# Performance work log

Hardware: AMD Instinct MI355X
Metric: run time of the kernel (lower is better)

Reference implementation:

```python
import jax, jax.numpy as jnp
import numpy as np
from jax import lax

H, W = 480, 640
EPS = 1e-20
DN = ('NCHW', 'OIHW', 'NCHW')


def _nconv(x, c, w_raw, b, pad):
    # Normalized convolution: positive weights via softplus (EnforcePos hook).
    w = jax.nn.softplus(w_raw)                     # (O, I, kh, kw)
    pads = [(pad, pad), (pad, pad)]
    denom = lax.conv_general_dilated(c, w, (1, 1), pads, dimension_numbers=DN)
    nomin = lax.conv_general_dilated(x * c, w, (1, 1), pads, dimension_numbers=DN)
    out = nomin / (denom + EPS) + b.reshape(1, -1, 1, 1)
    s = w.reshape(w.shape[0], -1).sum(-1).reshape(1, -1, 1, 1)  # per-out-ch weight sum
    return out, denom / s


def _pool2(x, c):
    # max_pool2d(c, 2, 2, return_indices=True) + gather of x at the argmax
    # locations (vectorized form of the per-(b,c) Python gather loops).
    B, C, h, w = c.shape
    cb = c.reshape(B, C, h // 2, 2, w // 2, 2).transpose(0, 1, 2, 4, 3, 5).reshape(B, C, h // 2, w // 2, 4)
    xb = x.reshape(B, C, h // 2, 2, w // 2, 2).transpose(0, 1, 2, 4, 3, 5).reshape(B, C, h // 2, w // 2, 4)
    idx = jnp.argmax(cb, axis=-1)
    c_ds = jnp.max(cb, axis=-1)
    x_ds = jnp.take_along_axis(xb, idx[..., None], axis=-1)[..., 0]
    return x_ds, c_ds


def _up2(a):
    return jnp.repeat(jnp.repeat(a, 2, axis=2), 2, axis=3)


def _adaptive_mat(n_in, n_out):
    # 1D adaptive average pooling as a (n_out, n_in) averaging matrix
    i = np.arange(n_out)
    st = (i * n_in) // n_out
    en = -((-(i + 1) * n_in) // n_out)  # ceil division
    M = np.zeros((n_out, n_in), np.float32)
    for r in range(n_out):
        M[r, st[r]:en[r]] = 1.0 / (en[r] - st[r])
    return jnp.asarray(M)


def _forward(S, w1, b1, w2, b2, w3, b3, w4, b4, w5, b5, w6, b6, w65, b65, w7, b7):
    c0 = (S > 0.01).astype(S.dtype)
    x1, c1 = _nconv(S, c0, w1, b1, 2)
    x1, c1 = _nconv(x1, c1, w2, b2, 2)
    x1, c1 = _nconv(x1, c1, w3, b3, 2)
    # scale 1/2
    x1_ds, c1_ds = _pool2(x1, c1)
    c1_ds = c1_ds / 4
    x2_ds, c2_ds = _nconv(x1_ds, c1_ds, w2, b2, 2)
    x2_ds, c2_ds = _nconv(x2_ds, c2_ds, w3, b3, 2)
    # scale 1/4
    x2_dss, c2_dss = _pool2(x2_ds, c2_ds)
    c2_dss = c2_dss / 4
    x3_ds, c3_ds = _nconv(x2_dss, c2_dss, w2, b2, 2)
    # scale 1/8
    x3_dss, c3_dss = _pool2(x3_ds, c3_ds)
    c3_dss = c3_dss / 4
    x4_ds, c4_ds = _nconv(x3_dss, c3_dss, w2, b2, 2)
    # decoder
    x4, c4 = _up2(x4_ds), _up2(c4_ds)
    x34_ds, c34_ds = _nconv(jnp.concatenate((x3_ds, x4), 1), jnp.concatenate((c3_ds, c4), 1), w4, b4, 1)
    x34, c34 = _up2(x34_ds), _up2(c34_ds)
    x23_ds, c23_ds = _nconv(jnp.concatenate((x2_ds, x34), 1), jnp.concatenate((c2_ds, c34), 1), w5, b5, 1)
    x23, c23 = _up2(x23_ds), _up2(c23_ds)
    xo, co = _nconv(jnp.concatenate((x23, x1), 1), jnp.concatenate((c23, c1), 1), w6, b6, 0)  # shrinks by 2
    xo, co = _nconv(xo, co, w65, b65, 1)
    xo, co = _nconv(xo, co, w7, b7, 0)
    Mh = _adaptive_mat(xo.shape[2], H)
    Mw = _adaptive_mat(xo.shape[3], W)
    return jnp.einsum('oi,bcij,pj->bcop', Mh, xo, Mw)


def setup_inputs() -> dict:
    key = jax.random.key(0)
    ks = jax.random.split(key, 20)
    B = 8
    d = {
        'fout': jax.random.normal(ks[0], (B, 3, H, W), jnp.float32),
        'S': jax.random.uniform(ks[1], (B, 1, H, W), jnp.float32),
        'K': jax.random.normal(ks[2], (B, 3, 3), jnp.float32),
    }
    shapes = {'w1': (4, 1, 5, 5), 'w2': (4, 4, 5, 5), 'w3': (4, 4, 5, 5),
              'w4': (4, 8, 3, 3), 'w5': (4, 8, 3, 3), 'w6': (4, 8, 3, 3),
              'w65': (4, 4, 3, 3), 'w7': (1, 4, 1, 1)}
    i = 3
    for name, sh in shapes.items():
        d[name] = 0.1 * jax.random.normal(ks[i], sh, jnp.float32)
        i += 1
        d['b' + name[1:]] = 0.01 * jax.random.normal(ks[i], (sh[0],), jnp.float32)
        i += 1
    return d


def reference(fout, S, K, w1, b1, w2, b2, w3, b3, w4, b4, w5, b5, w6, b6, w65, b65, w7, b7):
    # fout and K are accepted but unused by the original forward.
    return _forward(S, w1, b1, w2, b2, w3, b3, w4, b4, w5, b5, w6, b6, w65, b65, w7, b7)
```

## Files before the change

kernel.cpp:

```cpp
#include <hip/hip_runtime.h>


#define EPSN 1e-20f

typedef float v2f __attribute__((ext_vector_type(2)));

__device__ __forceinline__ float softplusf(float x) {
    return fmaxf(x, 0.f) + log1pf(expf(-fabsf(x)));
}
__device__ __forceinline__ float rcpf(float x) { return __builtin_amdgcn_rcpf(x); }

__device__ __forceinline__ void wsum4(const float4* s_w4, int n, int tid, float4* dst)
{
    if (tid < 64) {
        float4 a = make_float4(0.f, 0.f, 0.f, 0.f);
        for (int i = tid; i < n; i += 64) {
            float4 w = s_w4[i];
            a.x += w.x; a.y += w.y; a.z += w.z; a.w += w.w;
        }
        #pragma unroll
        for (int off = 32; off; off >>= 1) {
            a.x += __shfl_xor(a.x, off);
            a.y += __shfl_xor(a.y, off);
            a.z += __shfl_xor(a.z, off);
            a.w += __shfl_xor(a.w, off);
        }
        if (tid == 0) *dst = a;
    }
}

__device__ __forceinline__ void tap4(v2f v, v2f w01, v2f w23, v2f* a)
{
    asm("v_pk_fma_f32 %0, %1, %2, %0 op_sel:[0,0,0] op_sel_hi:[1,0,1]"
        : "+v"(a[0]) : "v"(w01), "v"(v));
    asm("v_pk_fma_f32 %0, %1, %2, %0 op_sel:[0,0,0] op_sel_hi:[1,0,1]"
        : "+v"(a[1]) : "v"(w23), "v"(v));
    asm("v_pk_fma_f32 %0, %1, %2, %0 op_sel:[0,1,0] op_sel_hi:[1,1,1]"
        : "+v"(a[2]) : "v"(w01), "v"(v));
    asm("v_pk_fma_f32 %0, %1, %2, %0 op_sel:[0,1,0] op_sel_hi:[1,1,1]"
        : "+v"(a[3]) : "v"(w23), "v"(v));
}
#define TAP2(W01, W23, VA, VB)  tap4((VA),(W01),(W23),aA); tap4((VB),(W01),(W23),aB);

#define NC_EPI(A, XO, CO)                                            \
    XO.x = A[2].x*rcpf(A[0].x+EPSN)+bias.x; CO.x = A[0].x*rs0;       \
    XO.y = A[2].y*rcpf(A[0].y+EPSN)+bias.y; CO.y = A[0].y*rs1;       \
    XO.z = A[3].x*rcpf(A[1].x+EPSN)+bias.z; CO.z = A[1].x*rs2;       \
    XO.w = A[3].y*rcpf(A[1].y+EPSN)+bias.w; CO.w = A[1].y*rs3;

#define NC_STORE_PACKED(HOUT, WOUT)                                         \
    {                                                                       \
        const int oh = oh0 + ty, ow = ow0 + 2 * tx;                         \
        if (oh < (HOUT) && ow < (WOUT)) {                                   \
            float4 bias = s_bias, ssum = s_sum;                             \
            float rs0=rcpf(ssum.x), rs1=rcpf(ssum.y),                       \
                  rs2=rcpf(ssum.z), rs3=rcpf(ssum.w);                       \
            size_t t = ((size_t)b * (HOUT) + oh) * (WOUT) + ow;             \
            float4 xo, co;                                                  \
            NC_EPI(aA, xo, co)                                              \
            xout4[t] = xo; cout4[t] = co;                                   \
            if (ow + 1 < (WOUT)) {                                          \
                NC_EPI(aB, xo, co)                                          \
                xout4[t+1] = xo; cout4[t+1] = co;                           \
            }                                                               \
        }                                                                   \
    }

__global__ __launch_bounds__(256) void nconv5_first(
    const float* __restrict__ S,
    const float* __restrict__ wraw, const float* __restrict__ braw,
    float4* __restrict__ xout4, float4* __restrict__ cout4,
    int Hh, int Ww)
{
    __shared__ v2f sdE[20][19], sdO[20][19];
    __shared__ float4 s_w4[25];
    __shared__ float4 s_sum, s_bias;
    const int b = blockIdx.z;
    const int oh0 = blockIdx.y * 16, ow0 = blockIdx.x * 32;
    const int tx = threadIdx.x, ty = threadIdx.y, tid = ty * 16 + tx;

    if (tid < 25) {
        float4 w;
        w.x = softplusf(wraw[tid]);      w.y = softplusf(wraw[25 + tid]);
        w.z = softplusf(wraw[50 + tid]); w.w = softplusf(wraw[75 + tid]);
        s_w4[tid] = w;
    }
    if (tid == 0) s_bias = make_float4(braw[0], braw[1], braw[2], braw[3]);
    __syncthreads();

    for (int i = tid; i < 20 * 18; i += 256) {
        int ly = i / 18, j = i - ly * 18;
        int ih = oh0 - 2 + ly, iw = ow0 - 2 + 2 * j;
        float s0 = 0.f, s1 = 0.f;
        if ((unsigned)ih < (unsigned)Hh && iw >= 0 && iw < Ww - 1) {
            float2 t = *(const float2*)&S[((size_t)b * Hh + ih) * Ww + iw];
            s0 = t.x; s1 = t.y;
        }
        float c0 = (s0 > 0.01f) ? 1.f : 0.f;
        float c1 = (s1 > 0.01f) ? 1.f : 0.f;
        sdE[ly][j] = (v2f){c0, s0 * c0};
        sdO[ly][j] = (v2f){c1, s1 * c1};
    }
    wsum4(s_w4, 25, tid, &s_sum);
    __syncthreads();

    v2f aA[4] = {}, aB[4] = {};
    #pragma unroll
    for (int kj = 0; kj < 5; ++kj) {
        const v2f* rE = &sdE[ty + kj][tx];
        const v2f* rO = &sdO[ty + kj][tx];
        v2f e0 = rE[0], o0 = rO[0], e1 = rE[1], o1 = rO[1], e2 = rE[2], o2 = rO[2];
        const v2f* wr = (const v2f*)&s_w4[kj * 5];
        TAP2(wr[0], wr[1], e0, o0)
        TAP2(wr[2], wr[3], o0, e1)
        TAP2(wr[4], wr[5], e1, o1)
        TAP2(wr[6], wr[7], o1, e2)
        TAP2(wr[8], wr[9], e2, o2)
    }
    NC_STORE_PACKED(Hh, Ww)
}

template<bool POOL>
__global__ __launch_bounds__(256) void nconv5p4(
    const float4* __restrict__ xin4, const float4* __restrict__ cin4,
    const float* __restrict__ wraw, const float* __restrict__ braw,
    float4* __restrict__ xout4, float4* __restrict__ cout4,
    float4* __restrict__ xo_p, float4* __restrict__ co_p,
    int Hh, int Ww)
{
    __shared__ v2f sdE[4][20][19], sdO[4][20][19];
    __shared__ float4 s_w4[100];
    __shared__ float4 s_sum, s_bias;
    const int b = blockIdx.z;
    const int oh0 = blockIdx.y * 16, ow0 = blockIdx.x * 32;
    const int tx = threadIdx.x, ty = threadIdx.y, tid = ty * 16 + tx;

    if (tid < 100) {
        float4 w;
        w.x = softplusf(wraw[tid]);       w.y = softplusf(wraw[100 + tid]);
        w.z = softplusf(wraw[200 + tid]); w.w = softplusf(wraw[300 + tid]);
        s_w4[tid] = w;
    }
    if (tid == 0) s_bias = make_float4(braw[0], braw[1], braw[2], braw[3]);
    __syncthreads();

    const float4 z = make_float4(0.f, 0.f, 0.f, 0.f);
    for (int i = tid; i < 20 * 18; i += 256) {
        int ly = i / 18, j = i - ly * 18;
        int ih = oh0 - 2 + ly, iw = ow0 - 2 + 2 * j;
        float4 cA = z, xA = z, cB = z, xB = z;
        if ((unsigned)ih < (unsigned)Hh) {
            size_t rb = ((size_t)b * Hh + ih) * Ww;
            if ((unsigned)iw < (unsigned)Ww)       { cA = cin4[rb + iw];     xA = xin4[rb + iw]; }
            if ((unsigned)(iw + 1) < (unsigned)Ww) { cB = cin4[rb + iw + 1]; xB = xin4[rb + iw + 1]; }
        }
        sdE[0][ly][j] = (v2f){cA.x, xA.x * cA.x};
        sdE[1][ly][j] = (v2f){cA.y, xA.y * cA.y};
        sdE[2][ly][j] = (v2f){cA.z, xA.z * cA.z};
        sdE[3][ly][j] = (v2f){cA.w, xA.w * cA.w};
        sdO[0][ly][j] = (v2f){cB.x, xB.x * cB.x};
        sdO[1][ly][j] = (v2f){cB.y, xB.y * cB.y};
        sdO[2][ly][j] = (v2f){cB.z, xB.z * cB.z};
        sdO[3][ly][j] = (v2f){cB.w, xB.w * cB.w};
    }
    wsum4(s_w4, 100, tid, &s_sum);
    __syncthreads();

    v2f aA[4] = {}, aB[4] = {};
    #pragma unroll 1
    for (int ci = 0; ci < 4; ++ci) {
        #pragma unroll
        for (int kj = 0; kj < 5; ++kj) {
            const v2f* rE = &sdE[ci][ty + kj][tx];
            const v2f* rO = &sdO[ci][ty + kj][tx];
            v2f e0 = rE[0], o0 = rO[0], e1 = rE[1], o1 = rO[1], e2 = rE[2], o2 = rO[2];
            const v2f* wr = (const v2f*)&s_w4[ci * 25 + kj * 5];
            TAP2(wr[0], wr[1], e0, o0)
            TAP2(wr[2], wr[3], o0, e1)
            TAP2(wr[4], wr[5], e1, o1)
            TAP2(wr[6], wr[7], o1, e2)
            TAP2(wr[8], wr[9], e2, o2)
        }
    }

    const int oh = oh0 + ty, ow = ow0 + 2 * tx;
    float4 bias = s_bias, ssum = s_sum;
    float rs0 = rcpf(ssum.x), rs1 = rcpf(ssum.y),
          rs2 = rcpf(ssum.z), rs3 = rcpf(ssum.w);
    float4 xoA, coA, xoB, coB;
    NC_EPI(aA, xoA, coA)
    NC_EPI(aB, xoB, coB)
    const bool rowok = oh < Hh, colA = ow < Ww, colB = ow + 1 < Ww;
    if (rowok && colA) {
        size_t t = ((size_t)b * Hh + oh) * Ww + ow;
        xout4[t] = xoA; cout4[t] = coA;
        if (colB) { xout4[t + 1] = xoB; cout4[t + 1] = coB; }
    }
    if (POOL) {
        float4 cb = coA, xb = xoA;
        if (coB.x > cb.x) { cb.x = coB.x; xb.x = xoB.x; }
        if (coB.y > cb.y) { cb.y = coB.y; xb.y = xoB.y; }
        if (coB.z > cb.z) { cb.z = coB.z; xb.z = xoB.z; }
        if (coB.w > cb.w) { cb.w = coB.w; xb.w = xoB.w; }
        float4 cb2, xb2;
        cb2.x = __shfl_down(cb.x, 16); xb2.x = __shfl_down(xb.x, 16);
        cb2.y = __shfl_down(cb.y, 16); xb2.y = __shfl_down(xb.y, 16);
        cb2.z = __shfl_down(cb.z, 16); xb2.z = __shfl_down(xb.z, 16);
        cb2.w = __shfl_down(cb.w, 16); xb2.w = __shfl_down(xb.w, 16);
        if (!(ty & 1) && rowok && colA) {
            if (cb2.x > cb.x) { cb.x = cb2.x; xb.x = xb2.x; }
            if (cb2.y > cb.y) { cb.y = cb2.y; xb.y = xb2.y; }
            if (cb2.z > cb.z) { cb.z = cb2.z; xb.z = xb2.z; }
            if (cb2.w > cb.w) { cb.w = cb2.w; xb.w = xb2.w; }
            cb.x *= 0.25f; cb.y *= 0.25f; cb.z *= 0.25f; cb.w *= 0.25f;
            size_t tp = ((size_t)b * (Hh >> 1) + (oh >> 1)) * (Ww >> 1) + (ow >> 1);
            xo_p[tp] = xb; co_p[tp] = cb;
        }
    }
}

template<bool UP_FIRST, int PAD>
__global__ __launch_bounds__(256) void nconv3cat(
    const float4* __restrict__ xd4, const float4* __restrict__ cd4,
    const float4* __restrict__ xu4, const float4* __restrict__ cu4,
    const float* __restrict__ wraw, const float* __restrict__ braw,
    float4* __restrict__ xout4, float4* __restrict__ cout4,
    int Hin, int Win)
{
    __shared__ v2f sdE[4][18][18], sdO[4][18][18];
    __shared__ v2f sup[4][10][19];
    __shared__ float4 s_w4[72];
    __shared__ float4 s_sum, s_bias;

    const int Hout = Hin - 2 + 2 * PAD, Wout = Win - 2 + 2 * PAD;
    const int Hu = Hin / 2, Wu = Win / 2;
    const int b = blockIdx.z;
    const int oh0 = blockIdx.y * 16, ow0 = blockIdx.x * 32;
    const int tx = threadIdx.x, ty = threadIdx.y, tid = ty * 16 + tx;

    if (tid < 72) {
        float4 w;
        w.x = softplusf(wraw[tid]);       w.y = softplusf(wraw[72 + tid]);
        w.z = softplusf(wraw[144 + tid]); w.w = softplusf(wraw[216 + tid]);
        s_w4[tid] = w;
    }
    if (tid == 0) s_bias = make_float4(braw[0], braw[1], braw[2], braw[3]);
    __syncthreads();

    const float4 z = make_float4(0.f, 0.f, 0.f, 0.f);
    for (int i = tid; i < 18 * 17; i += 256) {
        int ly = i / 17, j = i - ly * 17;
        int ih = oh0 - PAD + ly, iw = ow0 - PAD + 2 * j;
        float4 cA = z, xA = z, cB = z, xB = z;
        if ((unsigned)ih < (unsigned)Hin) {
            size_t rb = ((size_t)b * Hin + ih) * Win;
            if ((unsigned)iw < (unsigned)Win)       { cA = cd4[rb + iw];     xA = xd4[rb + iw]; }
            if ((unsigned)(iw + 1) < (unsigned)Win) { cB = cd4[rb + iw + 1]; xB = xd4[rb + iw + 1]; }
        }
        sdE[0][ly][j] = (v2f){cA.x, xA.x * cA.x};
        sdE[1][ly][j] = (v2f){cA.y, xA.y * cA.y};
        sdE[2][ly][j] = (v2f){cA.z, xA.z * cA.z};
        sdE[3][ly][j] = (v2f){cA.w, xA.w * cA.w};
        sdO[0][ly][j] = (v2f){cB.x, xB.x * cB.x};
        sdO[1][ly][j] = (v2f){cB.y, xB.y * cB.y};
        sdO[2][ly][j] = (v2f){cB.z, xB.z * cB.z};
        sdO[3][ly][j] = (v2f){cB.w, xB.w * cB.w};
    }
    const int ru0 = (oh0 - PAD) >> 1, cu0 = (ow0 - PAD) >> 1;
    for (int i = tid; i < 10 * 18; i += 256) {
        int r = i / 18, k = i - r * 18;
        int ur = ru0 + r, uc = cu0 + k;
        float4 cU = z, xU = z;
        if ((unsigned)ur < (unsigned)Hu && (unsigned)uc < (unsigned)Wu) {
            size_t t = ((size_t)b * Hu + ur) * Wu + uc;
            cU = cu4[t]; xU = xu4[t];
        }
        sup[0][r][k] = (v2f){cU.x, xU.x * cU.x};
        sup[1][r][k] = (v2f){cU.y, xU.y * cU.y};
        sup[2][r][k] = (v2f){cU.z, xU.z * cU.z};
        sup[3][r][k] = (v2f){cU.w, xU.w * cU.w};
    }
    wsum4(s_w4, 72, tid, &s_sum);
    __syncthreads();

    v2f aA[4] = {}, aB[4] = {};
    #pragma unroll 1
    for (int ci = 0; ci < 4; ++ci) {
        const int chD = UP_FIRST ? ci + 4 : ci;
        const int chU = UP_FIRST ? ci : ci + 4;
        #pragma unroll
        for (int kj = 0; kj < 3; ++kj) {
            const v2f* rE = &sdE[ci][ty + kj][tx];
            const v2f* rO = &sdO[ci][ty + kj][tx];
            v2f e0 = rE[0], o0 = rO[0], e1 = rE[1], o1 = rO[1];
            const v2f* wr = (const v2f*)&s_w4[chD * 9 + kj * 3];
            TAP2(wr[0], wr[1], e0, o0)
            TAP2(wr[2], wr[3], o0, e1)
            TAP2(wr[4], wr[5], e1, o1)
        }
        #pragma unroll
        for (int kj = 0; kj < 3; ++kj) {
            int lyu = (ty + kj + PAD) >> 1;
            const v2f* ru = &sup[ci][lyu][tx];
            v2f u0 = ru[0], u1 = ru[1];
            v2f q0, q1, q2, q3;
            if (PAD == 1) {
                v2f u2 = ru[2];
                q0 = u0; q1 = u1; q2 = u1; q3 = u2;
            } else {
                q0 = u0; q1 = u0; q2 = u1; q3 = u1;
            }
            const v2f* wr = (const v2f*)&s_w4[chU * 9 + kj * 3];
            TAP2(wr[0], wr[1], q0, q1)
            TAP2(wr[2], wr[3], q1, q2)
            TAP2(wr[4], wr[5], q2, q3)
        }
    }
    NC_STORE_PACKED(Hout, Wout)
}

__global__ __launch_bounds__(256) void nconv3p_w7(
    const float4* __restrict__ xin4, const float4* __restrict__ cin4,
    const float* __restrict__ wraw, const float* __restrict__ braw,
    const float* __restrict__ w7raw, const float* __restrict__ b7raw,
    float* __restrict__ zout,
    int Hh, int Ww)
{
    __shared__ v2f sdE[4][18][18], sdO[4][18][18];
    __shared__ float4 s_w4[36];
    __shared__ float4 s_sum, s_bias, s_w7;
    __shared__ float s_b7;
    const int b = blockIdx.z;
    const int oh0 = blockIdx.y * 16, ow0 = blockIdx.x * 32;
    const int tx = threadIdx.x, ty = threadIdx.y, tid = ty * 16 + tx;

    if (tid < 36) {
        float4 w;
        w.x = softplusf(wraw[tid]);      w.y = softplusf(wraw[36 + tid]);
        w.z = softplusf(wraw[72 + tid]); w.w = softplusf(wraw[108 + tid]);
        s_w4[tid] = w;
    }
    if (tid == 0) {
        s_bias = make_float4(braw[0], braw[1], braw[2], braw[3]);
        s_w7 = make_float4(softplusf(w7raw[0]), softplusf(w7raw[1]),
                           softplusf(w7raw[2]), softplusf(w7raw[3]));
        s_b7 = b7raw[0];
    }
    __syncthreads();

    const float4 z = make_float4(0.f, 0.f, 0.f, 0.f);
    for (int i = tid; i < 18 * 17; i += 256) {
        int ly = i / 17, j = i - ly * 17;
        int ih = oh0 - 1 + ly, iw = ow0 - 1 + 2 * j;
        float4 cA = z, xA = z, cB = z, xB = z;
        if ((unsigned)ih < (unsigned)Hh) {
            size_t rb = ((size_t)b * Hh + ih) * Ww;
            if ((unsigned)iw < (unsigned)Ww)       { cA = cin4[rb + iw];     xA = xin4[rb + iw]; }
            if ((unsigned)(iw + 1) < (unsigned)Ww) { cB = cin4[rb + iw + 1]; xB = xin4[rb + iw + 1]; }
        }
        sdE[0][ly][j] = (v2f){cA.x, xA.x * cA.x};
        sdE[1][ly][j] = (v2f){cA.y, xA.y * cA.y};
        sdE[2][ly][j] = (v2f){cA.z, xA.z * cA.z};
        sdE[3][ly][j] = (v2f){cA.w, xA.w * cA.w};
        sdO[0][ly][j] = (v2f){cB.x, xB.x * cB.x};
        sdO[1][ly][j] = (v2f){cB.y, xB.y * cB.y};
        sdO[2][ly][j] = (v2f){cB.z, xB.z * cB.z};
        sdO[3][ly][j] = (v2f){cB.w, xB.w * cB.w};
    }
    wsum4(s_w4, 36, tid, &s_sum);
    __syncthreads();

    v2f aA[4] = {}, aB[4] = {};
    #pragma unroll 1
    for (int ci = 0; ci < 4; ++ci) {
        #pragma unroll
        for (int kj = 0; kj < 3; ++kj) {
            const v2f* rE = &sdE[ci][ty + kj][tx];
            const v2f* rO = &sdO[ci][ty + kj][tx];
            v2f e0 = rE[0], o0 = rO[0], e1 = rE[1], o1 = rO[1];
            const v2f* wr = (const v2f*)&s_w4[ci * 9 + kj * 3];
            TAP2(wr[0], wr[1], e0, o0)
            TAP2(wr[2], wr[3], o0, e1)
            TAP2(wr[4], wr[5], e1, o1)
        }
    }

    const int oh = oh0 + ty, ow = ow0 + 2 * tx;
    if (oh >= Hh || ow >= Ww) return;
    float4 bias = s_bias, ssum = s_sum, w7 = s_w7;
    float b7 = s_b7;
    float rs0 = rcpf(ssum.x), rs1 = rcpf(ssum.y),
          rs2 = rcpf(ssum.z), rs3 = rcpf(ssum.w);
    float4 xo, co;
    NC_EPI(aA, xo, co)
    float den7 = w7.x * co.x + w7.y * co.y + w7.z * co.z + w7.w * co.w;
    float nom7 = w7.x * xo.x * co.x + w7.y * xo.y * co.y
               + w7.z * xo.z * co.z + w7.w * xo.w * co.w;
    float zA = nom7 * rcpf(den7 + EPSN) + b7;
    size_t t = ((size_t)b * Hh + oh) * Ww + ow;
    if (ow + 1 < Ww) {
        NC_EPI(aB, xo, co)
        den7 = w7.x * co.x + w7.y * co.y + w7.z * co.z + w7.w * co.w;
        nom7 = w7.x * xo.x * co.x + w7.y * xo.y * co.y
             + w7.z * xo.z * co.z + w7.w * xo.w * co.w;
        float zB = nom7 * rcpf(den7 + EPSN) + b7;
        *(float2*)&zout[t] = make_float2(zA, zB);
    } else {
        zout[t] = zA;
    }
}

__global__ __launch_bounds__(256) void apoolk(
    const float* __restrict__ in, float* __restrict__ out)
{
    const int HI = 478, WI = 638, HO = 480, WO = 640;
    int total = 8 * HO * WO;
    int i = blockIdx.x * 256 + threadIdx.x;
    if (i >= total) return;
    int ow = i % WO;
    int oh = (i / WO) % HO;
    int b  = i / (WO * HO);
    int sh = (oh * HI) / HO, eh = ((oh + 1) * HI + HO - 1) / HO;
    int sw = (ow * WI) / WO, ew = ((ow + 1) * WI + WO - 1) / WO;
    float s = 0.f;
    for (int ih = sh; ih < eh; ++ih)
        for (int iw = sw; iw < ew; ++iw)
            s += in[((size_t)b * HI + ih) * WI + iw];
    out[i] = s * rcpf((float)((eh - sh) * (ew - sw)));
}

extern "C" void kernel_launch(void* const* d_in, const int* in_sizes, int n_in,
                              void* d_out, int out_size, void* d_ws, size_t ws_size,
                              hipStream_t stream)
{
    const float* S   = (const float*)d_in[1];
    const float* w1  = (const float*)d_in[3];  const float* b1  = (const float*)d_in[4];
    const float* w2  = (const float*)d_in[5];  const float* b2  = (const float*)d_in[6];
    const float* w3  = (const float*)d_in[7];  const float* b3  = (const float*)d_in[8];
    const float* w4  = (const float*)d_in[9];  const float* b4  = (const float*)d_in[10];
    const float* w5  = (const float*)d_in[11]; const float* b5  = (const float*)d_in[12];
    const float* w6  = (const float*)d_in[13]; const float* b6  = (const float*)d_in[14];
    const float* w65 = (const float*)d_in[15]; const float* b65 = (const float*)d_in[16];
    const float* w7  = (const float*)d_in[17]; const float* b7  = (const float*)d_in[18];
    float* out = (float*)d_out;
    float* ws  = (float*)d_ws;

    const size_t FULL = 9830400, HALF = 2457600, QUAR = 614400, EIGH = 153600;
    float4 *A0 = (float4*)ws,              *A1 = (float4*)(ws + FULL),
           *A2 = (float4*)(ws + 2*FULL),   *A3 = (float4*)(ws + 3*FULL);
    float4 *P0 = (float4*)(ws + 4*FULL),            *P1 = (float4*)(ws + 4*FULL + HALF),
           *P2 = (float4*)(ws + 4*FULL + 2*HALF),   *P3 = (float4*)(ws + 4*FULL + 3*HALF);
    float4 *Q0 = (float4*)(ws + 4*FULL + 4*HALF),          *Q1 = (float4*)(ws + 4*FULL + 4*HALF + QUAR),
           *Q2 = (float4*)(ws + 4*FULL + 4*HALF + 2*QUAR), *Q3 = (float4*)(ws + 4*FULL + 4*HALF + 3*QUAR);
    float4 *E0 = (float4*)(ws + 4*FULL + 4*HALF + 4*QUAR),
           *E1 = (float4*)(ws + 4*FULL + 4*HALF + 4*QUAR + EIGH),
           *E2 = (float4*)(ws + 4*FULL + 4*HALF + 4*QUAR + 2*EIGH),
           *E3 = (float4*)(ws + 4*FULL + 4*HALF + 4*QUAR + 3*EIGH);

    dim3 blk(16, 16);
    auto grd = [](int Ho, int Wo) { return dim3((Wo + 31) / 32, (Ho + 15) / 16, 8); };

    nconv5_first<<<grd(480, 640), blk, 0, stream>>>(S, w1, b1, A0, A1, 480, 640);
    nconv5p4<false><<<grd(480, 640), blk, 0, stream>>>(A0, A1, w2, b2, A2, A3, nullptr, nullptr, 480, 640);
    nconv5p4<true ><<<grd(480, 640), blk, 0, stream>>>(A2, A3, w3, b3, A0, A1, P0, P1, 480, 640);
    nconv5p4<false><<<grd(240, 320), blk, 0, stream>>>(P0, P1, w2, b2, P2, P3, nullptr, nullptr, 240, 320);
    nconv5p4<true ><<<grd(240, 320), blk, 0, stream>>>(P2, P3, w3, b3, P0, P1, Q0, Q1, 240, 320);
    nconv5p4<true ><<<grd(120, 160), blk, 0, stream>>>(Q0, Q1, w2, b2, Q2, Q3, E0, E1, 120, 160);
    nconv5p4<false><<<grd(60, 80), blk, 0, stream>>>(E0, E1, w2, b2, E2, E3, nullptr, nullptr, 60, 80);
    nconv3cat<false, 1><<<grd(120, 160), blk, 0, stream>>>(Q2, Q3, E2, E3, w4, b4, Q0, Q1, 120, 160);
    nconv3cat<false, 1><<<grd(240, 320), blk, 0, stream>>>(P0, P1, Q0, Q1, w5, b5, P2, P3, 240, 320);
    nconv3cat<true , 0><<<grd(478, 638), blk, 0, stream>>>(A0, A1, P2, P3, w6, b6, A2, A3, 480, 640);
    nconv3p_w7<<<grd(478, 638), blk, 0, stream>>>(A2, A3, w65, b65, w7, b7, (float*)A0, 478, 638);
    apoolk<<<(8 * 480 * 640 + 255) / 256, 256, 0, stream>>>((float*)A0, out);
}
```

Measured before the change: 354.7 us.

## Fuse consecutive normalized convolutions into single kernels with halo recompute

Result: slower. 419.4 us (+18.2%).

```diff
diff --git a/kernel.cpp b/kernel.cpp
--- a/kernel.cpp
+++ b/kernel.cpp
@@ -42,6 +42,13 @@
 }
 #define TAP2(W01, W23, VA, VB)  tap4((VA),(W01),(W23),aA); tap4((VB),(W01),(W23),aB);
 
+#define MIDV(DEN, NOM, RS, BB, V) \
+    ((V) ? (v2f){(DEN)*(RS), ((NOM)*rcpf((DEN)+EPSN)+(BB))*((DEN)*(RS))} : (v2f){0.f, 0.f})
+
+#define NC_EPI(A, XO, CO)                                            \
+    XO.x = A[2].x*rcpf(A[0].x+EPSN)+bias.x; CO.x = A[0].x*rs0;       \
+    XO.y = A[2].y*rcpf(A[0].y+EPSN)+bias.y; CO.y = A[1].y... 
+#undef NC_EPI
 #define NC_EPI(A, XO, CO)                                            \
     XO.x = A[2].x*rcpf(A[0].x+EPSN)+bias.x; CO.x = A[0].x*rs0;       \
     XO.y = A[2].y*rcpf(A[0].y+EPSN)+bias.y; CO.y = A[0].y*rs1;       \
@@ -120,61 +127,158 @@
     NC_STORE_PACKED(Hh, Ww)
 }
 
-template<bool POOL>
-__global__ __launch_bounds__(256) void nconv5p4(
-    const float4* __restrict__ xin4, const float4* __restrict__ cin4,
-    const float* __restrict__ wraw, const float* __restrict__ braw,
-    float4* __restrict__ xout4, float4* __restrict__ cout4,
-    float4* __restrict__ xo_p, float4* __restrict__ co_p,
-    int Hh, int Ww)
-{
-    __shared__ v2f sdE[4][20][19], sdO[4][20][19];
-    __shared__ float4 s_w4[100];
-    __shared__ float4 s_sum, s_bias;
-    const int b = blockIdx.z;
-    const int oh0 = blockIdx.y * 16, ow0 = blockIdx.x * 32;
-    const int tx = threadIdx.x, ty = threadIdx.y, tid = ty * 16 + tx;
-
-    if (tid < 100) {
-        float4 w;
-        w.x = softplusf(wraw[tid]);       w.y = softplusf(wraw[100 + tid]);
-        w.z = softplusf(wraw[200 + tid]); w.w = softplusf(wraw[300 + tid]);
-        s_w4[tid] = w;
-    }
-    if (tid == 0) s_bias = make_float4(braw[0], braw[1], braw[2], braw[3]);
-    __syncthreads();
-
-    const float4 z = make_float4(0.f, 0.f, 0.f, 0.f);
-    for (int i = tid; i < 20 * 18; i += 256) {
-        int ly = i / 18, j = i - ly * 18;
-        int ih = oh0 - 2 + ly, iw = ow0 - 2 + 2 * j;
-        float4 cA = z, xA = z, cB = z, xB = z;
-        if ((unsigned)ih < (unsigned)Hh) {
-            size_t rb = ((size_t)b * Hh + ih) * Ww;
-            if ((unsigned)iw < (unsigned)Ww)       { cA = cin4[rb + iw];     xA = xin4[rb + iw]; }
-            if ((unsigned)(iw + 1) < (unsigned)Ww) { cB = cin4[rb + iw + 1]; xB = xin4[rb + iw + 1]; }
-        }
-        sdE[0][ly][j] = (v2f){cA.x, xA.x * cA.x};
-        sdE[1][ly][j] = (v2f){cA.y, xA.y * cA.y};
-        sdE[2][ly][j] = (v2f){cA.z, xA.z * cA.z};
-        sdE[3][ly][j] = (v2f){cA.w, xA.w * cA.w};
-        sdO[0][ly][j] = (v2f){cB.x, xB.x * cB.x};
-        sdO[1][ly][j] = (v2f){cB.y, xB.y * cB.y};
-        sdO[2][ly][j] = (v2f){cB.z, xB.z * cB.z};
-        sdO[3][ly][j] = (v2f){cB.w, xB.w * cB.w};
-    }
-    wsum4(s_w4, 100, tid, &s_sum);
-    __syncthreads();
-
+__device__ __forceinline__ void c5task(const v2f* sb, const float4* sw,
+                                       int mr, int mj, v2f* oA, v2f* oB)
+{
     v2f aA[4] = {}, aB[4] = {};
     #pragma unroll 1
     for (int ci = 0; ci < 4; ++ci) {
         #pragma unroll
         for (int kj = 0; kj < 5; ++kj) {
-            const v2f* rE = &sdE[ci][ty + kj][tx];
-            const v2f* rO = &sdO[ci][ty + kj][tx];
+            const v2f* rE = &sb[(ci * 24 + mr + kj) * 20 + mj];
+            const v2f* rO = &sb[1920 + (ci * 24 + mr + kj) * 20 + mj];
             v2f e0 = rE[0], o0 = rO[0], e1 = rE[1], o1 = rO[1], e2 = rE[2], o2 = rO[2];
-            const v2f* wr = (const v2f*)&s_w4[ci * 25 + kj * 5];
+            const v2f* wr = (const v2f*)&sw[ci * 25 + kj * 5];
+            TAP2(wr[0], wr[1], e0, o0)
+            TAP2(wr[2], wr[3], o0, e1)
+            TAP2(wr[4], wr[5], e1, o1)
+            TAP2(wr[6], wr[7], o1, e2)
+            TAP2(wr[8], wr[9], e2, o2)
+        }
+    }
+    oA[0] = aA[0]; oA[1] = aA[1]; oA[2] = aA[2]; oA[3] = aA[3];
+    oB[0] = aB[0]; oB[1] = aB[1]; oB[2] = aB[2]; oB[3] = aB[3];
+}
+
+template<bool POOL>
+__global__ __launch_bounds__(256) void nconv5x2(
+    const float4* __restrict__ xin4, const float4* __restrict__ cin4,
+    const float* __restrict__ w2raw, const float* __restrict__ b2raw,
+    const float* __restrict__ w3raw, const float* __restrict__ b3raw,
+    float4* __restrict__ xout4, float4* __restrict__ cout4,
+    float4* __restrict__ xo_p, float4* __restrict__ co_p,
+    int Hh, int Ww)
+{
+    __shared__ v2f sbuf[3840];
+    __shared__ float4 s_w2[100], s_w3[100];
+    __shared__ float4 s_sum2, s_b2f, s_sum, s_bias;
+    const int b = blockIdx.z;
+    const int oh0 = blockIdx.y * 16, ow0 = blockIdx.x * 32;
+    const int tx = threadIdx.x, ty = threadIdx.y, tid = ty * 16 + tx;
+
+    if (tid < 100) {
+        float4 w;
+        w.x = softplusf(w2raw[tid]);       w.y = softplusf(w2raw[100 + tid]);
+        w.z = softplusf(w2raw[200 + tid]); w.w = softplusf(w2raw[300 + tid]);
+        s_w2[tid] = w;
+        w.x = softplusf(w3raw[tid]);       w.y = softplusf(w3raw[100 + tid]);
+        w.z = softplusf(w3raw[200 + tid]); w.w = softplusf(w3raw[300 + tid]);
+        s_w3[tid] = w;
+    }
+    if (tid == 0) {
+        s_b2f  = make_float4(b2raw[0], b2raw[1], b2raw[2], b2raw[3]);
+        s_bias = make_float4(b3raw[0], b3raw[1], b3raw[2], b3raw[3]);
+    }
+    __syncthreads();
+
+    const float4 z4 = make_float4(0.f, 0.f, 0.f, 0.f);
+    for (int i = tid; i < 24 * 20; i += 256) {
+        int ly = i / 20, j = i - ly * 20;
+        int ih = oh0 - 4 + ly, iw = ow0 - 4 + 2 * j;
+        float4 cA = z4, xA = z4, cB = z4, xB = z4;
+        if ((unsigned)ih < (unsigned)Hh) {
+            size_t rb = ((size_t)b * Hh + ih) * Ww;
+            if ((unsigned)iw < (unsigned)Ww)       { cA = cin4[rb + iw];     xA = xin4[rb + iw]; }
+            if ((unsigned)(iw + 1) < (unsigned)Ww) { cB = cin4[rb + iw + 1]; xB = xin4[rb + iw + 1]; }
+        }
+        sbuf[(0 * 24 + ly) * 20 + j] = (v2f){cA.x, xA.x * cA.x};
+        sbuf[(1 * 24 + ly) * 20 + j] = (v2f){cA.y, xA.y * cA.y};
+        sbuf[(2 * 24 + ly) * 20 + j] = (v2f){cA.z, xA.z * cA.z};
+        sbuf[(3 * 24 + ly) * 20 + j] = (v2f){cA.w, xA.w * cA.w};
+        sbuf[1920 + (0 * 24 + ly) * 20 + j] = (v2f){cB.x, xB.x * cB.x};
+        sbuf[1920 + (1 * 24 + ly) * 20 + j] = (v2f){cB.y, xB.y * cB.y};
+        sbuf[1920 + (2 * 24 + ly) * 20 + j] = (v2f){cB.z, xB.z * cB.z};
+        sbuf[1920 + (3 * 24 + ly) * 20 + j] = (v2f){cB.w, xB.w * cB.w};
+    }
+    wsum4(s_w2, 100, tid, &s_sum2);
+    wsum4(s_w3, 100, tid, &s_sum);
+    __syncthreads();
+
+    v2f k0[8], k1[8];
+    const bool t1ok = tid < 104;
+    {
+        v2f qA[4], qB[4];
+        int mr = tid / 18, mj = tid - (tid / 18) * 18;
+        c5task(sbuf, s_w2, mr, mj, qA, qB);
+        float4 b2 = s_b2f, sm = s_sum2;
+        float rs0 = rcpf(sm.x), rs1 = rcpf(sm.y), rs2 = rcpf(sm.z), rs3 = rcpf(sm.w);
+        int gr = oh0 - 2 + mr, gc = ow0 - 2 + 2 * mj;
+        bool vA = (unsigned)gr < (unsigned)Hh && (unsigned)gc < (unsigned)Ww;
+        bool vB = (unsigned)gr < (unsigned)Hh && (unsigned)(gc + 1) < (unsigned)Ww;
+        k0[0] = MIDV(qA[0].x, qA[2].x, rs0, b2.x, vA);
+        k0[1] = MIDV(qA[0].y, qA[2].y, rs1, b2.y, vA);
+        k0[2] = MIDV(qA[1].x, qA[3].x, rs2, b2.z, vA);
+        k0[3] = MIDV(qA[1].y, qA[3].y, rs3, b2.w, vA);
+        k0[4] = MIDV(qB[0].x, qB[2].x, rs0, b2.x, vB);
+        k0[5] = MIDV(qB[0].y, qB[2].y, rs1, b2.y, vB);
+        k0[6] = MIDV(qB[1].x, qB[3].x, rs2, b2.z, vB);
+        k0[7] = MIDV(qB[1].y, qB[3].y, rs3, b2.w, vB);
+    }
+    if (t1ok) {
+        v2f qA[4], qB[4];
+        int t = tid + 256;
+        int mr = t / 18, mj = t - (t / 18) * 18;
+        c5task(sbuf, s_w2, mr, mj, qA, qB);
+        float4 b2 = s_b2f, sm = s_sum2;
+        float rs0 = rcpf(sm.x), rs1 = rcpf(sm.y), rs2 = rcpf(sm.z), rs3 = rcpf(sm.w);
+        int gr = oh0 - 2 + mr, gc = ow0 - 2 + 2 * mj;
+        bool vA = (unsigned)gr < (unsigned)Hh && (unsigned)gc < (unsigned)Ww;
+        bool vB = (unsigned)gr < (unsigned)Hh && (unsigned)(gc + 1) < (unsigned)Ww;
+        k1[0] = MIDV(qA[0].x, qA[2].x, rs0, b2.x, vA);
+        k1[1] = MIDV(qA[0].y, qA[2].y, rs1, b2.y, vA);
+        k1[2] = MIDV(qA[1].x, qA[3].x, rs2, b2.z, vA);
+        k1[3] = MIDV(qA[1].y, qA[3].y, rs3, b2.w, vA);
+        k1[4] = MIDV(qB[0].x, qB[2].x, rs0, b2.x, vB);
+        k1[5] = MIDV(qB[0].y, qB[2].y, rs1, b2.y, vB);
+        k1[6] = MIDV(qB[1].x, qB[3].x, rs2, b2.z, vB);
+        k1[7] = MIDV(qB[1].y, qB[3].y, rs3, b2.w, vB);
+    }
+    __syncthreads();
+
+    {
+        int mr = tid / 18, mj = tid - (tid / 18) * 18;
+        sbuf[(0 * 20 + mr) * 18 + mj] = k0[0];
+        sbuf[(1 * 20 + mr) * 18 + mj] = k0[1];
+        sbuf[(2 * 20 + mr) * 18 + mj] = k0[2];
+        sbuf[(3 * 20 + mr) * 18 + mj] = k0[3];
+        sbuf[1440 + (0 * 20 + mr) * 18 + mj] = k0[4];
+        sbuf[1440 + (1 * 20 + mr) * 18 + mj] = k0[5];
+        sbuf[1440 + (2 * 20 + mr) * 18 + mj] = k0[6];
+        sbuf[1440 + (3 * 20 + mr) * 18 + mj] = k0[7];
+    }
+    if (t1ok) {
+        int t = tid + 256;
+        int mr = t / 18, mj = t - (t / 18) * 18;
+        sbuf[(0 * 20 + mr) * 18 + mj] = k1[0];
+        sbuf[(1 * 20 + mr) * 18 + mj] = k1[1];
+        sbuf[(2 * 20 + mr) * 18 + mj] = k1[2];
+        sbuf[(3 * 20 + mr) * 18 + mj] = k1[3];
+        sbuf[1440 + (0 * 20 + mr) * 18 + mj] = k1[4];
+        sbuf[1440 + (1 * 20 + mr) * 18 + mj] = k1[5];
+        sbuf[1440 + (2 * 20 + mr) * 18 + mj] = k1[6];
+        sbuf[1440 + (3 * 20 + mr) * 18 + mj] = k1[7];
+    }
+    __syncthreads();
+
+    v2f aA[4] = {}, aB[4] = {};
+    #pragma unroll 1
+    for (int ci = 0; ci < 4; ++ci) {
+        #pragma unroll
+        for (int kj = 0; kj < 5; ++kj) {
+            const v2f* rE = &sbuf[(ci * 20 + ty + kj) * 18 + tx];
+            const v2f* rO = &sbuf[1440 + (ci * 20 + ty + kj) * 18 + tx];
+            v2f e0 = rE[0], o0 = rO[0], e1 = rE[1], o1 = rO[1], e2 = rE[2], o2 = rO[2];
+            const v2f* wr = (const v2f*)&s_w3[ci * 25 + kj * 5];
             TAP2(wr[0], wr[1], e0, o0)
             TAP2(wr[2], wr[3], o0, e1)
             TAP2(wr[4], wr[5], e1, o1)
@@ -219,6 +323,105 @@
     }
 }
 
+template<bool POOL>
+__global__ __launch_bounds__(256) void nconv5p4(
+    const float4* __restrict__ xin4, const float4* __restrict__ cin4,
+    const float* __restrict__ wraw, const float* __restrict__ braw,
+    float4* __restrict__ xout4, float4* __restrict__ cout4,
+    float4* __restrict__ xo_p, float4* __restrict__ co_p,
+    int Hh, int Ww)
+{
+    __shared__ v2f sdE[4][20][19], sdO[4][20][19];
+    __shared__ float4 s_w4[100];
+    __shared__ float4 s_sum, s_bias;
+    const int b = blockIdx.z;
+    const int oh0 = blockIdx.y * 16, ow0 = blockIdx.x * 32;
+    const int tx = threadIdx.x, ty = threadIdx.y, tid = ty * 16 + tx;
+
+    if (tid < 100) {
+        float4 w;
+        w.x = softplusf(wraw[tid]);       w.y = softplusf(wraw[100 + tid]);
+        w.z = softplusf(wraw[200 + tid]); w.w = softplusf(wraw[300 + tid]);
+        s_w4[tid] = w;
+    }
+    if (tid == 0) s_bias = make_float4(braw[0], braw[1], braw[2], braw[3]);
+    __syncthreads();
+
+    const float4 z = make_float4(0.f, 0.f, 0.f, 0.f);
+    for (int i = tid; i < 20 * 18; i += 256) {
+        int ly = i / 18, j = i - ly * 18;
+        int ih = oh0 - 2 + ly, iw = ow0 - 2 + 2 * j;
+        float4 cA = z, xA = z, cB = z, xB = z;
+        if ((unsigned)ih < (unsigned)Hh) {
+            size_t rb = ((size_t)b * Hh + ih) * Ww;
+            if ((unsigned)iw < (unsigned)Ww)       { cA = cin4[rb + iw];     xA = xin4[rb + iw]; }
+            if ((unsigned)(iw + 1) < (unsigned)Ww) { cB = cin4[rb + iw + 1]; xB = xin4[rb + iw + 1]; }
+        }
+        sdE[0][ly][j] = (v2f){cA.x, xA.x * cA.x};
+        sdE[1][ly][j] = (v2f){cA.y, xA.y * cA.y};
+        sdE[2][ly][j] = (v2f){cA.z, xA.z * cA.z};
+        sdE[3][ly][j] = (v2f){cA.w, xA.w * cA.w};
+        sdO[0][ly][j] = (v2f){cB.x, xB.x * cB.x};
+        sdO[1][ly][j] = (v2f){cB.y, xB.y * cB.y};
+        sdO[2][ly][j] = (v2f){cB.z, xB.z * cB.z};
+        sdO[3][ly][j] = (v2f){cB.w, xB.w * cB.w};
+    }
+    wsum4(s_w4, 100, tid, &s_sum);
+    __syncthreads();
+
+    v2f aA[4] = {}, aB[4] = {};
+    #pragma unroll 1
+    for (int ci = 0; ci < 4; ++ci) {
+        #pragma unroll
+        for (int kj = 0; kj < 5; ++kj) {
+            const v2f* rE = &sdE[ci][ty + kj][tx];
+            const v2f* rO = &sdO[ci][ty + kj][tx];
+            v2f e0 = rE[0], o0 = rO[0], e1 = rE[1], o1 = rO[1], e2 = rE[2], o2 = rO[2];
+            const v2f* wr = (const v2f*)&s_w4[ci * 25 + kj * 5];
+            TAP2(wr[0], wr[1], e0, o0)
+            TAP2(wr[2], wr[3], o0, e1)
+            TAP2(wr[4], wr[5], e1, o1)
+            TAP2(wr[6], wr[7], o1, e2)
+            TAP2(wr[8], wr[9], e2, o2)
+        }
+    }
+
+    const int oh = oh0 + ty, ow = ow0 + 2 * tx;
+    float4 bias = s_bias, ssum = s_sum;
+    float rs0 = rcpf(ssum.x), rs1 = rcpf(ssum.y),
+          rs2 = rcpf(ssum.z), rs3 = rcpf(ssum.w);
+    float4 xoA, coA, xoB, coB;
+    NC_EPI(aA, xoA, coA)
+    NC_EPI(aB, xoB, coB)
+    const bool rowok = oh < Hh, colA = ow < Ww, colB = ow + 1 < Ww;
+    if (rowok && colA) {
+        size_t t = ((size_t)b * Hh + oh) * Ww + ow;
+        xout4[t] = xoA; cout4[t] = coA;
+        if (colB) { xout4[t + 1] = xoB; cout4[t + 1] = coB; }
+    }
+    if (POOL) {
+        float4 cb = coA, xb = xoA;
+        if (coB.x > cb.x) { cb.x = coB.x; xb.x = xoB.x; }
+        if (coB.y > cb.y) { cb.y = coB.y; xb.y = xoB.y; }
+        if (coB.z > cb.z) { cb.z = coB.z; xb.z = xoB.z; }
+        if (coB.w > cb.w) { cb.w = coB.w; xb.w = xoB.w; }
+        float4 cb2, xb2;
+        cb2.x = __shfl_down(cb.x, 16); xb2.x = __shfl_down(xb.x, 16);
+        cb2.y = __shfl_down(cb.y, 16); xb2.y = __shfl_down(xb.y, 16);
+        cb2.z = __shfl_down(cb.z, 16); xb2.z = __shfl_down(xb.z, 16);
+        cb2.w = __shfl_down(cb.w, 16); xb2.w = __shfl_down(xb.w, 16);
+        if (!(ty & 1) && rowok && colA) {
+            if (cb2.x > cb.x) { cb.x = cb2.x; xb.x = xb2.x; }
+            if (cb2.y > cb.y) { cb.y = cb2.y; xb.y = xb2.y; }
+            if (cb2.z > cb.z) { cb.z = cb2.z; xb.z = xb2.z; }
+            if (cb2.w > cb.w) { cb.w = cb2.w; xb.w = xb2.w; }
+            cb.x *= 0.25f; cb.y *= 0.25f; cb.z *= 0.25f; cb.w *= 0.25f;
+            size_t tp = ((size_t)b * (Hh >> 1) + (oh >> 1)) * (Ww >> 1) + (ow >> 1);
+            xo_p[tp] = xb; co_p[tp] = cb;
+        }
+    }
+}
+
 template<bool UP_FIRST, int PAD>
 __global__ __launch_bounds__(256) void nconv3cat(
     const float4* __restrict__ xd4, const float4* __restrict__ cd4,
@@ -316,58 +519,157 @@
             TAP2(wr[4], wr[5], q2, q3)
         }
     }
+    size_t planeO; (void)planeO;
     NC_STORE_PACKED(Hout, Wout)
 }
 
-__global__ __launch_bounds__(256) void nconv3p_w7(
-    const float4* __restrict__ xin4, const float4* __restrict__ cin4,
-    const float* __restrict__ wraw, const float* __restrict__ braw,
+__global__ __launch_bounds__(256) void dtail(
+    const float4* __restrict__ xd4, const float4* __restrict__ cd4,
+    const float4* __restrict__ xu4, const float4* __restrict__ cu4,
+    const float* __restrict__ w6raw, const float* __restrict__ b6raw,
+    const float* __restrict__ w65raw, const float* __restrict__ b65raw,
     const float* __restrict__ w7raw, const float* __restrict__ b7raw,
-    float* __restrict__ zout,
-    int Hh, int Ww)
-{
-    __shared__ v2f sdE[4][18][18], sdO[4][18][18];
-    __shared__ float4 s_w4[36];
-    __shared__ float4 s_sum, s_bias, s_w7;
+    float* __restrict__ zout)
+{
+    __shared__ v2f sb[3920];
+    __shared__ float4 s_w6[72], s_w65[36];
+    __shared__ float4 s_sum6, s_b6f, s_sum, s_bias, s_w7v;
     __shared__ float s_b7;
+    const int H = 480, W = 640, HZ = 478, WZ = 638, HU = 240, WU = 320;
     const int b = blockIdx.z;
     const int oh0 = blockIdx.y * 16, ow0 = blockIdx.x * 32;
     const int tx = threadIdx.x, ty = threadIdx.y, tid = ty * 16 + tx;
 
-    if (tid < 36) {
+    if (tid < 72) {
         float4 w;
-        w.x = softplusf(wraw[tid]);      w.y = softplusf(wraw[36 + tid]);
-        w.z = softplusf(wraw[72 + tid]); w.w = softplusf(wraw[108 + tid]);
-        s_w4[tid] = w;
+        w.x = softplusf(w6raw[tid]);       w.y = softplusf(w6raw[72 + tid]);
+        w.z = softplusf(w6raw[144 + tid]); w.w = softplusf(w6raw[216 + tid]);
+        s_w6[tid] = w;
+    }
+    if (tid >= 128 && tid < 164) {
+        int i = tid - 128;
+        float4 w;
+        w.x = softplusf(w65raw[i]);      w.y = softplusf(w65raw[36 + i]);
+        w.z = softplusf(w65raw[72 + i]); w.w = softplusf(w65raw[108 + i]);
+        s_w65[i] = w;
     }
     if (tid == 0) {
-        s_bias = make_float4(braw[0], braw[1], braw[2], braw[3]);
-        s_w7 = make_float4(softplusf(w7raw[0]), softplusf(w7raw[1]),
-                           softplusf(w7raw[2]), softplusf(w7raw[3]));
+        s_b6f  = make_float4(b6raw[0], b6raw[1], b6raw[2], b6raw[3]);
+        s_bias = make_float4(b65raw[0], b65raw[1], b65raw[2], b65raw[3]);
+        s_w7v  = make_float4(softplusf(w7raw[0]), softplusf(w7raw[1]),
+                             softplusf(w7raw[2]), softplusf(w7raw[3]));
         s_b7 = b7raw[0];
     }
     __syncthreads();
 
-    const float4 z = make_float4(0.f, 0.f, 0.f, 0.f);
-    for (int i = tid; i < 18 * 17; i += 256) {
-        int ly = i / 17, j = i - ly * 17;
+    const float4 z4 = make_float4(0.f, 0.f, 0.f, 0.f);
+    for (int i = tid; i < 20 * 19; i += 256) {
+        int ly = i / 19, j = i - ly * 19;
         int ih = oh0 - 1 + ly, iw = ow0 - 1 + 2 * j;
-        float4 cA = z, xA = z, cB = z, xB = z;
-        if ((unsigned)ih < (unsigned)Hh) {
-            size_t rb = ((size_t)b * Hh + ih) * Ww;
-            if ((unsigned)iw < (unsigned)Ww)       { cA = cin4[rb + iw];     xA = xin4[rb + iw]; }
-            if ((unsigned)(iw + 1) < (unsigned)Ww) { cB = cin4[rb + iw + 1]; xB = xin4[rb + iw + 1]; }
-        }
-        sdE[0][ly][j] = (v2f){cA.x, xA.x * cA.x};
-        sdE[1][ly][j] = (v2f){cA.y, xA.y * cA.y};
-        sdE[2][ly][j] = (v2f){cA.z, xA.z * cA.z};
-        sdE[3][ly][j] = (v2f){cA.w, xA.w * cA.w};
-        sdO[0][ly][j] = (v2f){cB.x, xB.x * cB.x};
-        sdO[1][ly][j] = (v2f){cB.y, xB.y * cB.y};
-        sdO[2][ly][j] = (v2f){cB.z, xB.z * cB.z};
-        sdO[3][ly][j] = (v2f){cB.w, xB.w * cB.w};
-    }
-    wsum4(s_w4, 36, tid, &s_sum);
+        float4 cA = z4, xA = z4, cB = z4, xB = z4;
+        if ((unsigned)ih < (unsigned)H) {
+            size_t rb = ((size_t)b * H + ih) * W;
+            if ((unsigned)iw < (unsigned)W)       { cA = cd4[rb + iw];     xA = xd4[rb + iw]; }
+            if ((unsigned)(iw + 1) < (unsigned)W) { cB = cd4[rb + iw + 1]; xB = xd4[rb + iw + 1]; }
+        }
+        sb[(0 * 20 + ly) * 19 + j] = (v2f){cA.x, xA.x * cA.x};
+        sb[(1 * 20 + ly) * 19 + j] = (v2f){cA.y, xA.y * cA.y};
+        sb[(2 * 20 + ly) * 19 + j] = (v2f){cA.z, xA.z * cA.z};
+        sb[(3 * 20 + ly) * 19 + j] = (v2f){cA.w, xA.w * cA.w};
+        sb[1520 + (0 * 20 + ly) * 19 + j] = (v2f){cB.x, xB.x * cB.x};
+        sb[1520 + (1 * 20 + ly) * 19 + j] = (v2f){cB.y, xB.y * cB.y};
+        sb[1520 + (2 * 20 + ly) * 19 + j] = (v2f){cB.z, xB.z * cB.z};
+        sb[1520 + (3 * 20 + ly) * 19 + j] = (v2f){cB.w, xB.w * cB.w};
+    }
+    const int ru0 = (oh0 - 1) >> 1, cu0 = (ow0 - 1) >> 1;
+    for (int i = tid; i < 11 * 20; i += 256) {
+        int r = i / 20, k = i - r * 20;
+        int ur = ru0 + r, uc = cu0 + k;
+        float4 cU = z4, xU = z4;
+        if ((unsigned)ur < (unsigned)HU && (unsigned)uc < (unsigned)WU) {
+            size_t t = ((size_t)b * HU + ur) * WU + uc;
+            cU = cu4[t]; xU = xu4[t];
+        }
+        sb[3040 + (0 * 11 + r) * 20 + k] = (v2f){cU.x, xU.x * cU.x};
+        sb[3040 + (1 * 11 + r) * 20 + k] = (v2f){cU.y, xU.y * cU.y};
+        sb[3040 + (2 * 11 + r) * 20 + k] = (v2f){cU.z, xU.z * cU.z};
+        sb[3040 + (3 * 11 + r) * 20 + k] = (v2f){cU.w, xU.w * cU.w};
+    }
+    wsum4(s_w6, 72, tid, &s_sum6);
+    wsum4(s_w65, 36, tid, &s_sum);
+    __syncthreads();
+
+    v2f k0[8], k1[8];
+    const bool t1ok = tid < 50;
+    #pragma unroll 1
+    for (int tpass = 0; tpass < 2; ++tpass) {
+        if (tpass == 1 && !t1ok) break;
+        int t = tpass ? tid + 256 : tid;
+        int mr = t / 17, mj = t - (t / 17) * 17;
+        v2f aA[4] = {}, aB[4] = {};
+        #pragma unroll 1
+        for (int ci = 0; ci < 4; ++ci) {
+            #pragma unroll
+            for (int kj = 0; kj < 3; ++kj) {
+                const v2f* rE = &sb[(ci * 20 + mr + kj) * 19 + mj];
+                const v2f* rO = &sb[1520 + (ci * 20 + mr + kj) * 19 + mj];
+                v2f e0 = rE[0], o0 = rO[0], e1 = rE[1], o1 = rO[1];
+                const v2f* wr = (const v2f*)&s_w6[(ci + 4) * 9 + kj * 3];
+                TAP2(wr[0], wr[1], e0, o0)
+                TAP2(wr[2], wr[3], o0, e1)
+                TAP2(wr[4], wr[5], e1, o1)
+            }
+            #pragma unroll
+            for (int kj = 0; kj < 3; ++kj) {
+                int lyu = ((mr + kj - 1) >> 1) + 1;
+                const v2f* ru = &sb[3040 + (ci * 11 + lyu) * 20 + mj];
+                v2f u0 = ru[0], u1 = ru[1], u2 = ru[2];
+                const v2f* wr = (const v2f*)&s_w6[ci * 9 + kj * 3];
+                TAP2(wr[0], wr[1], u0, u1)
+                TAP2(wr[2], wr[3], u1, u1)
+                TAP2(wr[4], wr[5], u1, u2)
+            }
+        }
+        float4 b6 = s_b6f, sm = s_sum6;
+        float rs0 = rcpf(sm.x), rs1 = rcpf(sm.y), rs2 = rcpf(sm.z), rs3 = rcpf(sm.w);
+        int gr = oh0 - 1 + mr, gc = ow0 - 1 + 2 * mj;
+        bool vA = (unsigned)gr < (unsigned)HZ && (unsigned)gc < (unsigned)WZ;
+        bool vB = (unsigned)gr < (unsigned)HZ && (unsigned)(gc + 1) < (unsigned)WZ;
+        v2f* k = tpass ? k1 : k0;
+        k[0] = MIDV(aA[0].x, aA[2].x, rs0, b6.x, vA);
+        k[1] = MIDV(aA[0].y, aA[2].y, rs1, b6.y, vA);
+        k[2] = MIDV(aA[1].x, aA[3].x, rs2, b6.z, vA);
+        k[3] = MIDV(aA[1].y, aA[3].y, rs3, b6.w, vA);
+        k[4] = MIDV(aB[0].x, aB[2].x, rs0, b6.x, vB);
+        k[5] = MIDV(aB[0].y, aB[2].y, rs1, b6.y, vB);
+        k[6] = MIDV(aB[1].x, aB[3].x, rs2, b6.z, vB);
+        k[7] = MIDV(aB[1].y, aB[3].y, rs3, b6.w, vB);
+    }
+    __syncthreads();
+
+    {
+        int mr = tid / 17, mj = tid - (tid / 17) * 17;
+        sb[(0 * 18 + mr) * 17 + mj] = k0[0];
+        sb[(1 * 18 + mr) * 17 + mj] = k0[1];
+        sb[(2 * 18 + mr) * 17 + mj] = k0[2];
+        sb[(3 * 18 + mr) * 17 + mj] = k0[3];
+        sb[1224 + (0 * 18 + mr) * 17 + mj] = k0[4];
+        sb[1224 + (1 * 18 + mr) * 17 + mj] = k0[5];
+        sb[1224 + (2 * 18 + mr) * 17 + mj] = k0[6];
+        sb[1224 + (3 * 18 + mr) * 17 + mj] = k0[7];
+    }
+    if (t1ok) {
+        int t = tid + 256;
+        int mr = t / 17, mj = t - (t / 17) * 17;
+        sb[(0 * 18 + mr) * 17 + mj] = k1[0];
+        sb[(1 * 18 + mr) * 17 + mj] = k1[1];
+        sb[(2 * 18 + mr) * 17 + mj] = k1[2];
+        sb[(3 * 18 + mr) * 17 + mj] = k1[3];
+        sb[1224 + (0 * 18 + mr) * 17 + mj] = k1[4];
+        sb[1224 + (1 * 18 + mr) * 17 + mj] = k1[5];
+        sb[1224 + (2 * 18 + mr) * 17 + mj] = k1[6];
+        sb[1224 + (3 * 18 + mr) * 17 + mj] = k1[7];
+    }
     __syncthreads();
 
     v2f aA[4] = {}, aB[4] = {};
@@ -375,19 +677,18 @@
     for (int ci = 0; ci < 4; ++ci) {
         #pragma unroll
         for (int kj = 0; kj < 3; ++kj) {
-            const v2f* rE = &sdE[ci][ty + kj][tx];
-            const v2f* rO = &sdO[ci][ty + kj][tx];
+            const v2f* rE = &sb[(ci * 18 + ty + kj) * 17 + tx];
+            const v2f* rO = &sb[1224 + (ci * 18 + ty + kj) * 17 + tx];
             v2f e0 = rE[0], o0 = rO[0], e1 = rE[1], o1 = rO[1];
-            const v2f* wr = (const v2f*)&s_w4[ci * 9 + kj * 3];
+            const v2f* wr = (const v2f*)&s_w65[ci * 9 + kj * 3];
             TAP2(wr[0], wr[1], e0, o0)
             TAP2(wr[2], wr[3], o0, e1)
             TAP2(wr[4], wr[5], e1, o1)
         }
     }
-
     const int oh = oh0 + ty, ow = ow0 + 2 * tx;
-    if (oh >= Hh || ow >= Ww) return;
-    float4 bias = s_bias, ssum = s_sum, w7 = s_w7;
+    if (oh >= HZ || ow >= WZ) return;
+    float4 bias = s_bias, ssum = s_sum, w7 = s_w7v;
     float b7 = s_b7;
     float rs0 = rcpf(ssum.x), rs1 = rcpf(ssum.y),
           rs2 = rcpf(ssum.z), rs3 = rcpf(ssum.w);
@@ -397,8 +698,8 @@
     float nom7 = w7.x * xo.x * co.x + w7.y * xo.y * co.y
                + w7.z * xo.z * co.z + w7.w * xo.w * co.w;
     float zA = nom7 * rcpf(den7 + EPSN) + b7;
-    size_t t = ((size_t)b * Hh + oh) * Ww + ow;
-    if (ow + 1 < Ww) {
+    size_t t = ((size_t)b * HZ + oh) * WZ + ow;
+    if (ow + 1 < WZ) {
         NC_EPI(aB, xo, co)
         den7 = w7.x * co.x + w7.y * co.y + w7.z * co.z + w7.w * co.w;
         nom7 = w7.x * xo.x * co.x + w7.y * xo.y * co.y
@@ -461,15 +762,12 @@
     auto grd = [](int Ho, int Wo) { return dim3((Wo + 31) / 32, (Ho + 15) / 16, 8); };
 
     nconv5_first<<<grd(480, 640), blk, 0, stream>>>(S, w1, b1, A0, A1, 480, 640);
-    nconv5p4<false><<<grd(480, 640), blk, 0, stream>>>(A0, A1, w2, b2, A2, A3, nullptr, nullptr, 480, 640);
-    nconv5p4<true ><<<grd(480, 640), blk, 0, stream>>>(A2, A3, w3, b3, A0, A1, P0, P1, 480, 640);
-    nconv5p4<false><<<grd(240, 320), blk, 0, stream>>>(P0, P1, w2, b2, P2, P3, nullptr, nullptr, 240, 320);
-    nconv5p4<true ><<<grd(240, 320), blk, 0, stream>>>(P2, P3, w3, b3, P0, P1, Q0, Q1, 240, 320);
+    nconv5x2<true ><<<grd(480, 640), blk, 0, stream>>>(A0, A1, w2, b2, w3, b3, A2, A3, P0, P1, 480, 640);
+    nconv5x2<true ><<<grd(240, 320), blk, 0, stream>>>(P0, P1, w2, b2, w3, b3, P2, P3, Q0, Q1, 240, 320);
     nconv5p4<true ><<<grd(120, 160), blk, 0, stream>>>(Q0, Q1, w2, b2, Q2, Q3, E0, E1, 120, 160);
-    nconv5p4<false><<<grd(60, 80), blk, 0, stream>>>(E0, E1, w2, b2, E2, E3, nullptr, nullptr, 60, 80);
+    nconv5p4<false><<<grd(60, 80),   blk, 0, stream>>>(E0, E1, w2, b2, E2, E3, nullptr, nullptr, 60, 80);
     nconv3cat<false, 1><<<grd(120, 160), blk, 0, stream>>>(Q2, Q3, E2, E3, w4, b4, Q0, Q1, 120, 160);
-    nconv3cat<false, 1><<<grd(240, 320), blk, 0, stream>>>(P0, P1, Q0, Q1, w5, b5, P2, P3, 240, 320);
-    nconv3cat<true , 0><<<grd(478, 638), blk, 0, stream>>>(A0, A1, P2, P3, w6, b6, A2, A3, 480, 640);
-    nconv3p_w7<<<grd(478, 638), blk, 0, stream>>>(A2, A3, w65, b65, w7, b7, (float*)A0, 478, 638);
+    nconv3cat<false, 1><<<grd(240, 320), blk, 0, stream>>>(P2, P3, Q0, Q1, w5, b5, P0, P1, 240, 320);
+    dtail<<<grd(478, 638), blk, 0, stream>>>(A2, A3, P0, P1, w6, b6, w65, b65, w7, b7, (float*)A0);
     apoolk<<<(8 * 480 * 640 + 255) / 256, 256, 0, stream>>>((float*)A0, out);
 }
```
